# Kernel tuning notes

Hardware: AMD Instinct MI355X
Metric: run time of the kernel (lower is better)

Reference implementation:

```python
import jax, jax.numpy as jnp
import numpy as np

B, D, H, F, L, M, MEM, ACT, STO, HID = 2048, 1024, 8, 4096, 2, 256, 16, 32, 1024, 1024
HD = D // H
SCALE = HD ** -0.5
EPS = 1e-4


def rmsnorm(x, w):
    return x * jax.lax.rsqrt(jnp.mean(x * x, axis=-1, keepdims=True) + EPS) * w


def setup_inputs() -> dict:
    key = jax.random.key(0)
    ks = iter(jax.random.split(key, 32))

    def nrm(shape, scale=0.02):
        return jax.random.normal(next(ks), shape, dtype=jnp.float32) * scale

    return {
        'stoch': jax.random.normal(next(ks), (B, STO), dtype=jnp.float32),
        'deter': jax.random.normal(next(ks), (B, D), dtype=jnp.float32),
        'action': jax.random.normal(next(ks), (B, ACT), dtype=jnp.float32),
        'memory': jax.random.normal(next(ks), (B, MEM, D), dtype=jnp.float32),
        'inp_w1': nrm((STO + ACT, HID)), 'inp_b1': jnp.zeros((HID,), jnp.float32),
        'inp_nw': jnp.ones((HID,), jnp.float32),
        'inp_w2': nrm((HID, D)), 'inp_b2': jnp.zeros((D,), jnp.float32),
        'Wq': nrm((L, D, D)), 'bq': jnp.zeros((L, D), jnp.float32),
        'Wk': nrm((L, D, D)), 'bk': jnp.zeros((L, D), jnp.float32),
        'Wv': nrm((L, D, D)), 'bv': jnp.zeros((L, D), jnp.float32),
        'Wo': nrm((L, D, D)), 'bo': jnp.zeros((L, D), jnp.float32),
        'rel_emb': nrm((L, 2 * M + 1, H)),
        'n1w': jnp.ones((L, D), jnp.float32), 'n2w': jnp.ones((L, D), jnp.float32),
        'ffw1': nrm((L, D, F)), 'ffb1': jnp.zeros((L, F), jnp.float32),
        'ffw2': nrm((L, F, D)), 'ffb2': jnp.zeros((L, D), jnp.float32),
        'fnw': jnp.ones((D,), jnp.float32),
    }


def reference(stoch, deter, action, memory, inp_w1, inp_b1, inp_nw, inp_w2, inp_b2,
              Wq, bq, Wk, bk, Wv, bv, Wo, bo, rel_emb, n1w, n2w,
              ffw1, ffb1, ffw2, ffb2, fnw):
    # action normalization: denominator is detached in torch
    a = action / jax.lax.stop_gradient(jnp.maximum(jnp.abs(action), 1.0))
    tok = jnp.concatenate([stoch.reshape(stoch.shape[0], -1), a], axis=-1)
    tok = jax.nn.silu(rmsnorm(tok @ inp_w1 + inp_b1, inp_nw)) @ inp_w2 + inp_b2  # [B,D]
    seq = jnp.concatenate([memory, tok[:, None, :]], axis=1)  # [B,S,D], S = MEM+1
    S = seq.shape[1]
    rel = jnp.clip(jnp.arange(S)[:, None] - jnp.arange(S)[None, :], -M, M) + M  # [S,S]
    for l in range(L):
        xn = rmsnorm(seq, n1w[l])
        q = (xn @ Wq[l] + bq[l]).reshape(-1, S, H, HD)
        k = (xn @ Wk[l] + bk[l]).reshape(-1, S, H, HD)
        v = (xn @ Wv[l] + bv[l]).reshape(-1, S, H, HD)
        bias = rel_emb[l][rel].transpose(2, 0, 1)  # [H,S,S]
        scores = jnp.einsum('bqhd,bkhd->bhqk', q, k) * SCALE + bias[None]
        probs = jax.nn.softmax(scores, axis=-1)
        att = jnp.einsum('bhqk,bkhd->bqhd', probs, v).reshape(-1, S, D)
        seq = seq + (att @ Wo[l] + bo[l])
        xn2 = rmsnorm(seq, n2w[l])
        seq = seq + (jax.nn.gelu(xn2 @ ffw1[l] + ffb1[l], approximate=False) @ ffw2[l] + ffb2[l])
    new_deter = rmsnorm(seq[:, -1] + deter, fnw)
    new_mem = jax.lax.stop_gradient(seq[:, -MEM:])
    return (new_deter, new_mem)
```

## Files before the change

### kernel.cpp

```cpp
#include <hip/hip_runtime.h>
#include <hip/hip_bf16.h>
#include <math.h>

#define NB 2048
#define ND 1024
#define NH 8
#define NHD 128
#define NF 4096
#define NL 2
#define NMEM 16
#define NS 17
#define NROWS (NB*NS)
#define NTOK 1056
#define SCALE_ATT 0.08838834764831845f

typedef unsigned short u16;
typedef unsigned int u32;

typedef __bf16 bf16x8 __attribute__((ext_vector_type(8)));
typedef float f32x4 __attribute__((ext_vector_type(4)));

__device__ __forceinline__ float bf2f(u16 h) {
  union { u32 u; float f; } c; c.u = ((u32)h) << 16; return c.f;
}
__device__ __forceinline__ u16 f2bf(float f) {
  union { float ff; u32 u; } c; c.ff = f;
  return (u16)((c.u + 0x7FFFu + ((c.u >> 16) & 1u)) >> 16);
}
__device__ __forceinline__ bf16x8 as_b8(uint4 u) {
  union { uint4 u; bf16x8 b; } c; c.u = u; return c.b;
}

__device__ __forceinline__ void gload16(const void* g, void* l) {
  __builtin_amdgcn_global_load_lds(
      (const __attribute__((address_space(1))) void*)(uintptr_t)g,
      (__attribute__((address_space(3))) void*)(u32)(uintptr_t)l,
      16, 0, 0);
}

__device__ __forceinline__ void pack_tile(const float* __restrict__ src,
                                          u16* __restrict__ dst,
                                          int K, int N, int n0, int k0,
                                          float* tile )
{
  int tx = threadIdx.x & 31, ty = threadIdx.x >> 5;
#pragma unroll
  for (int r = ty; r < 32; r += 8)
    tile[r * 33 + tx] = src[(size_t)(k0 + r) * N + n0 + tx];
  __syncthreads();
#pragma unroll
  for (int r = ty; r < 32; r += 8)
    dst[(size_t)(n0 + r) * K + k0 + tx] = f2bf(tile[tx * 33 + r]);
}

__global__ __launch_bounds__(256)
void pack_wT_k(const float* __restrict__ src, u16* __restrict__ dst, int K, int N)
{
  __shared__ float tile[32 * 33];
  pack_tile(src, dst, K, N, blockIdx.x * 32, blockIdx.y * 32, tile);
}

__global__ __launch_bounds__(256)
void pack_layer_k(const float* __restrict__ wq, const float* __restrict__ wk,
                  const float* __restrict__ wv, const float* __restrict__ wo,
                  const float* __restrict__ w1, const float* __restrict__ w2,
                  const float* __restrict__ bq, const float* __restrict__ bk,
                  const float* __restrict__ bv,
                  u16* __restrict__ qkvT, u16* __restrict__ oT,
                  u16* __restrict__ f1T, u16* __restrict__ f2T,
                  float* __restrict__ BQKV)
{
  __shared__ float tile[32 * 33];
  int id = blockIdx.x;
  if (id < 4096) {
    int which = id >> 10, l = id & 1023;
    const float* src = which == 0 ? wq : which == 1 ? wk : which == 2 ? wv : wo;
    u16* dst = which == 3 ? oT : qkvT + (size_t)which * 1048576;
    pack_tile(src, dst, 1024, 1024, (l & 31) * 32, (l >> 5) * 32, tile);
  } else if (id < 8192) {
    int l = id - 4096;
    pack_tile(w1, f1T, 1024, 4096, (l & 127) * 32, (l >> 7) * 32, tile);
  } else if (id < 12288) {
    int l = id - 8192;
    pack_tile(w2, f2T, 4096, 1024, (l & 31) * 32, (l >> 5) * 32, tile);
  } else {
    int j = (id - 12288) * 256 + threadIdx.x;
    if (j < 3072)
      BQKV[j] = (j < 1024) ? bq[j] : (j < 2048 ? bk[j - 1024] : bv[j - 2048]);
  }
}

template<int EPI>
__global__ __launch_bounds__(256)
void gemm2_k(const u16* __restrict__ A, int lda,
             const u16* __restrict__ BT, int ldb,
             const float* __restrict__ bias,
             u16* __restrict__ Cb, float* __restrict__ Cf, int ldc,
             int K)
{
  __shared__ __align__(16) u16 Asm[2][128 * 32];
  __shared__ __align__(16) u16 Bsm[2][128 * 32];
  const int tid  = threadIdx.x;
  const int lane = tid & 63;
  const int wv   = tid >> 6;
  const int wm   = wv >> 1, wn = wv & 1;
  const int lr   = lane & 15;
  const int kb   = lane >> 4;

  const int gx = gridDim.x;
  const int nwg = gx * gridDim.y;
  int bid = blockIdx.y * gx + blockIdx.x;
  if ((nwg & 7) == 0) bid = (bid & 7) * (nwg >> 3) + (bid >> 3);
  const int bx = bid % gx, by = bid / gx;
  const long bmBase = (long)by * 128;
  const int  bnBase = bx * 128;

  const int srow = tid >> 2;
  const int skc  = ((tid & 3) ^ ((srow >> 1) & 3)) * 8;
  const u16* aG0 = A  + (size_t)(bmBase + srow) * lda + skc;
  const u16* aG1 = aG0 + (size_t)64 * lda;
  const u16* bG0 = BT + (size_t)(bnBase + srow) * ldb + skc;
  const u16* bG1 = bG0 + (size_t)64 * ldb;
  const int wbase = (tid & ~63) * 8;
  const int rslot = (kb ^ ((lr >> 1) & 3)) * 8;

  f32x4 acc[4][4];
#pragma unroll
  for (int m = 0; m < 4; ++m)
#pragma unroll
    for (int n = 0; n < 4; ++n)
      acc[m][n] = (f32x4){0.0f, 0.0f, 0.0f, 0.0f};

  const int nk = K >> 5;
  {
    u16* aL = &Asm[0][wbase];
    u16* bL = &Bsm[0][wbase];
    gload16(aG0, aL);
    gload16(aG1, aL + 2048);
    gload16(bG0, bL);
    gload16(bG1, bL + 2048);
  }
  asm volatile("s_waitcnt vmcnt(0)" ::: "memory");
  __builtin_amdgcn_s_barrier();

  for (int i = 0; i < nk; ++i) {
    const int cur = i & 1;
    if (i + 1 < nk) {
      const int kt = (i + 1) << 5;
      u16* aL = &Asm[cur ^ 1][wbase];
      u16* bL = &Bsm[cur ^ 1][wbase];
      gload16(aG0 + kt, aL);
      gload16(aG1 + kt, aL + 2048);
      gload16(bG0 + kt, bL);
      gload16(bG1 + kt, bL + 2048);
    }
    bf16x8 af[4], bfv[4];
#pragma unroll
    for (int m = 0; m < 4; ++m)
      af[m] = as_b8(*(const uint4*)&Asm[cur][(wm * 64 + m * 16 + lr) * 32 + rslot]);
#pragma unroll
    for (int n = 0; n < 4; ++n)
      bfv[n] = as_b8(*(const uint4*)&Bsm[cur][(wn * 64 + n * 16 + lr) * 32 + rslot]);
#pragma unroll
    for (int m = 0; m < 4; ++m)
#pragma unroll
      for (int n = 0; n < 4; ++n)
        acc[m][n] = __builtin_amdgcn_mfma_f32_16x16x32_bf16(af[m], bfv[n], acc[m][n], 0, 0, 0);
    asm volatile("s_waitcnt vmcnt(0)" ::: "memory");
    __builtin_amdgcn_s_barrier();
  }

#pragma unroll
  for (int m = 0; m < 4; ++m) {
#pragma unroll
    for (int n = 0; n < 4; ++n) {
      int gcol = bnBase + wn * 64 + n * 16 + lr;
      float bv = bias[gcol];
      long growb = bmBase + wm * 64 + m * 16 + (lane >> 4) * 4;
#pragma unroll
      for (int i = 0; i < 4; ++i) {
        float val = acc[m][n][i] + bv;
        long row = growb + i;
        if (EPI == 1) val = 0.5f * val * (1.0f + erff(val * 0.70710678118654752f));
        if (EPI == 0 || EPI == 1) {
          Cb[(size_t)row * ldc + gcol] = f2bf(val);
        } else if (EPI == 2) {
          float* p = Cf + (size_t)row * ldc + gcol;
          *p = *p + val;
        } else {
          Cf[(size_t)row * ldc + gcol] = val;
        }
      }
    }
  }
}

__global__ __launch_bounds__(256)
void prep_tokcat_k(const float* __restrict__ stoch, const float* __restrict__ action,
                   u16* __restrict__ tok)
{
  size_t idx = (size_t)blockIdx.x * 256 + threadIdx.x;
  if (idx >= (size_t)NB * NTOK) return;
  int b = (int)(idx / NTOK), j = (int)(idx % NTOK);
  float v;
  if (j < 1024) {
    v = stoch[(size_t)b * 1024 + j];
  } else {
    float a = action[(size_t)b * 32 + (j - 1024)];
    v = a / fmaxf(fabsf(a), 1.0f);
  }
  tok[idx] = f2bf(v);
}

__global__ __launch_bounds__(256)
void rmsnorm_f32_k(const float* __restrict__ X, const float* __restrict__ w,
                   u16* __restrict__ Y)
{
  const int wv = threadIdx.x >> 6, lane = threadIdx.x & 63;
  const size_t row = (size_t)blockIdx.x * 4 + wv;
  const float* x = X + row * 1024 + lane * 16;
  float4 v[4];
#pragma unroll
  for (int j = 0; j < 4; ++j) v[j] = ((const float4*)x)[j];
  float ss = 0.0f;
#pragma unroll
  for (int j = 0; j < 4; ++j)
    ss += v[j].x * v[j].x + v[j].y * v[j].y + v[j].z * v[j].z + v[j].w * v[j].w;
#pragma unroll
  for (int o = 1; o < 64; o <<= 1) ss += __shfl_xor(ss, o, 64);
  const float r = rsqrtf(ss * (1.0f / 1024.0f) + 1e-4f);
  const float* wp = w + lane * 16;
  union { u16 s[16]; uint4 u[2]; } ob;
#pragma unroll
  for (int j = 0; j < 4; ++j) {
    float4 wj = ((const float4*)wp)[j];
    ob.s[j * 4 + 0] = f2bf(v[j].x * r * wj.x);
    ob.s[j * 4 + 1] = f2bf(v[j].y * r * wj.y);
    ob.s[j * 4 + 2] = f2bf(v[j].z * r * wj.z);
    ob.s[j * 4 + 3] = f2bf(v[j].w * r * wj.w);
  }
  uint4* dst = (uint4*)(Y + row * 1024 + lane * 16);
  dst[0] = ob.u[0];
  dst[1] = ob.u[1];
}

__global__ __launch_bounds__(256)
void rmsnorm_silu_k(u16* __restrict__ X, const float* __restrict__ w)
{
  const int wv = threadIdx.x >> 6, lane = threadIdx.x & 63;
  const size_t row = (size_t)blockIdx.x * 4 + wv;
  u16* x = X + row * 1024 + lane * 16;
  union { u16 s[16]; uint4 u[2]; } iv;
  iv.u[0] = ((const uint4*)x)[0];
  iv.u[1] = ((const uint4*)x)[1];
  float f[16];
  float ss = 0.0f;
#pragma unroll
  for (int j = 0; j < 16; ++j) { f[j] = bf2f(iv.s[j]); ss += f[j] * f[j]; }
#pragma unroll
  for (int o = 1; o < 64; o <<= 1) ss += __shfl_xor(ss, o, 64);
  const float r = rsqrtf(ss * (1.0f / 1024.0f) + 1e-4f);
  const float* wp = w + lane * 16;
  union { u16 s[16]; uint4 u[2]; } ob;
#pragma unroll
  for (int j = 0; j < 16; ++j) {
    float n = f[j] * r * wp[j];
    ob.s[j] = f2bf(n / (1.0f + expf(-n)));
  }
  ((uint4*)x)[0] = ob.u[0];
  ((uint4*)x)[1] = ob.u[1];
}

__global__ __launch_bounds__(256)
void init_seq_k(const float* __restrict__ mem, float* __restrict__ seq)
{
  size_t idx = ((size_t)blockIdx.x * 256 + threadIdx.x) * 4;
  if (idx >= (size_t)NB * 16 * 1024) return;
  size_t b = idx / (16 * 1024), rem = idx % (16 * 1024);
  float4 v = *(const float4*)&mem[idx];
  *(float4*)&seq[b * (size_t)NS * 1024 + rem] = v;
}

__global__ __launch_bounds__(256)
void copy_mem_k(const float* __restrict__ seq, float* __restrict__ out)
{
  size_t idx = ((size_t)blockIdx.x * 256 + threadIdx.x) * 4;
  if (idx >= (size_t)NB * 16 * 1024) return;
  size_t b = idx / (16 * 1024), rem = idx % (16 * 1024);
  float4 v = *(const float4*)&seq[b * (size_t)NS * 1024 + 1024 + rem];
  *(float4*)&out[idx] = v;
}

__global__ __launch_bounds__(256)
void final_deter_k(const float* __restrict__ seq, const float* __restrict__ deter,
                   const float* __restrict__ fnw, float* __restrict__ out)
{
  int b = blockIdx.x;
  const float* xs = seq + ((size_t)b * NS + 16) * 1024;
  const float* dt = deter + (size_t)b * 1024;
  int t = threadIdx.x;
  float v[4];
#pragma unroll
  for (int j = 0; j < 4; ++j) v[j] = xs[t * 4 + j] + dt[t * 4 + j];
  float ss = v[0] * v[0] + v[1] * v[1] + v[2] * v[2] + v[3] * v[3];
#pragma unroll
  for (int o = 1; o < 64; o <<= 1) ss += __shfl_xor(ss, o, 64);
  __shared__ float red[4];
  if ((t & 63) == 0) red[t >> 6] = ss;
  __syncthreads();
  float tot = red[0] + red[1] + red[2] + red[3];
  float r = rsqrtf(tot * (1.0f / 1024.0f) + 1e-4f);
  float4 ov;
  ov.x = v[0] * r * fnw[t * 4 + 0];
  ov.y = v[1] * r * fnw[t * 4 + 1];
  ov.z = v[2] * r * fnw[t * 4 + 2];
  ov.w = v[3] * r * fnw[t * 4 + 3];
  *(float4*)&out[(size_t)b * 1024 + t * 4] = ov;
}

#define LSTR 132
__global__ __launch_bounds__(256)
void attn_k(const u16* __restrict__ QKV, const float* __restrict__ rel,
            u16* __restrict__ O)
{
  __shared__ float qs[NS * LSTR];
  __shared__ float ks[NS * LSTR];
  __shared__ float vs[NS * LSTR];
  __shared__ float sc[NS * 20];
  int bh = blockIdx.x;
  int b = bh >> 3, h = bh & 7;
  int t = threadIdx.x;
  const size_t rowb = (size_t)b * NS * 3072 + h * 128;
  for (int e = t; e < NS * 16; e += 256) {
    int i = e >> 4, d = (e & 15) * 8;
    size_t off = rowb + (size_t)i * 3072 + d;
    uint4 q4 = *(const uint4*)(QKV + off);
    uint4 k4 = *(const uint4*)(QKV + off + 1024);
    uint4 v4 = *(const uint4*)(QKV + off + 2048);
    const u16* qp = (const u16*)&q4;
    const u16* kp = (const u16*)&k4;
    const u16* vp = (const u16*)&v4;
#pragma unroll
    for (int j = 0; j < 8; ++j) {
      qs[i * LSTR + d + j] = bf2f(qp[j]);
      ks[i * LSTR + d + j] = bf2f(kp[j]);
      vs[i * LSTR + d + j] = bf2f(vp[j]);
    }
  }
  __syncthreads();
  for (int e = t; e < NS * NS; e += 256) {
    int i = e / NS, j = e % NS;
    const float4* q4 = (const float4*)&qs[i * LSTR];
    const float4* k4 = (const float4*)&ks[j * LSTR];
    float s = 0.0f;
#pragma unroll
    for (int dd = 0; dd < 32; ++dd) {
      float4 a = q4[dd], bb = k4[dd];
      s += a.x * bb.x + a.y * bb.y + a.z * bb.z + a.w * bb.w;
    }
    sc[i * 20 + j] = s * SCALE_ATT + rel[(i - j + 256) * 8 + h];
  }
  __syncthreads();
  if (t < NS) {
    float mx = -1e30f;
    for (int j = 0; j < NS; ++j) mx = fmaxf(mx, sc[t * 20 + j]);
    float sum = 0.0f;
    for (int j = 0; j < NS; ++j) { float e = expf(sc[t * 20 + j] - mx); sc[t * 20 + j] = e; sum += e; }
    float inv = 1.0f / sum;
    for (int j = 0; j < NS; ++j) sc[t * 20 + j] *= inv;
  }
  __syncthreads();
  const size_t obase = (size_t)b * NS * 1024 + h * 128;
  for (int e = t; e < NS * 128; e += 256) {
    int i = e >> 7, d = e & 127;
    float o = 0.0f;
#pragma unroll
    for (int j = 0; j < NS; ++j) o += sc[i * 20 + j] * vs[j * LSTR + d];
    O[obase + (size_t)i * 1024 + d] = f2bf(o);
  }
}

extern "C" void kernel_launch(void* const* d_in, const int* in_sizes, int n_in,
                              void* d_out, int out_size, void* d_ws, size_t ws_size,
                              hipStream_t stream)
{
  const float* stoch  = (const float*)d_in[0];
  const float* deter  = (const float*)d_in[1];
  const float* action = (const float*)d_in[2];
  const float* memory = (const float*)d_in[3];
  const float* inp_w1 = (const float*)d_in[4];
  const float* inp_b1 = (const float*)d_in[5];
  const float* inp_nw = (const float*)d_in[6];
  const float* inp_w2 = (const float*)d_in[7];
  const float* inp_b2 = (const float*)d_in[8];
  const float* Wq = (const float*)d_in[9];
  const float* bq = (const float*)d_in[10];
  const float* Wk = (const float*)d_in[11];
  const float* bk = (const float*)d_in[12];
  const float* Wv = (const float*)d_in[13];
  const float* bv = (const float*)d_in[14];
  const float* Wo = (const float*)d_in[15];
  const float* bo = (const float*)d_in[16];
  const float* rel_emb = (const float*)d_in[17];
  const float* n1w = (const float*)d_in[18];
  const float* n2w = (const float*)d_in[19];
  const float* ffw1 = (const float*)d_in[20];
  const float* ffb1 = (const float*)d_in[21];
  const float* ffw2 = (const float*)d_in[22];
  const float* ffb2 = (const float*)d_in[23];
  const float* fnw  = (const float*)d_in[24];
  float* out = (float*)d_out;

  char* ws = (char*)d_ws;
  float* SEQ = (float*)ws;
  u16* XN  = (u16*)(ws + 142606336ULL);
  u16* QKV = (u16*)(ws + 213909504ULL);
  u16* FFH = QKV;
  u16* TOK = (u16*)(ws + 427819008ULL);
  u16* H1  = (u16*)(ws + 432144384ULL);
  u16* PK  = (u16*)(ws + 436338688ULL);
  float* BQKV = (float*)(ws + 461504512ULL);
  if (ws_size < 461516800ULL) return;

  dim3 blk(256);

  u16* w1T = PK;
  u16* w2T = PK + 1024 * 1056;
  pack_wT_k<<<dim3(1024 / 32, 1056 / 32), blk, 0, stream>>>(inp_w1, w1T, NTOK, 1024);
  pack_wT_k<<<dim3(1024 / 32, 1024 / 32), blk, 0, stream>>>(inp_w2, w2T, 1024, 1024);
  prep_tokcat_k<<<(NB * NTOK + 255) / 256, blk, 0, stream>>>(stoch, action, TOK);
  gemm2_k<0><<<dim3(8, 16), blk, 0, stream>>>(TOK, NTOK, w1T, NTOK, inp_b1, H1, nullptr, 1024, NTOK);
  rmsnorm_silu_k<<<NB / 4, blk, 0, stream>>>(H1, inp_nw);
  gemm2_k<3><<<dim3(8, 16), blk, 0, stream>>>(H1, 1024, w2T, 1024, inp_b2, nullptr, SEQ + 16 * 1024, NS * 1024, 1024);
  init_seq_k<<<(NB * 16 * 1024 / 4 + 255) / 256, blk, 0, stream>>>(memory, SEQ);

  u16* qkvT = PK;
  u16* oT  = PK + 3145728;
  u16* f1T = PK + 4194304;
  u16* f2T = PK + 8388608;

  for (int l = 0; l < NL; ++l) {
    const float* wq = Wq + (size_t)l * ND * ND;
    const float* wk = Wk + (size_t)l * ND * ND;
    const float* wv = Wv + (size_t)l * ND * ND;
    const float* wo = Wo + (size_t)l * ND * ND;
    const float* w1 = ffw1 + (size_t)l * ND * NF;
    const float* w2 = ffw2 + (size_t)l * NF * ND;
    const float* rl = rel_emb + (size_t)l * 513 * NH;

    pack_layer_k<<<12300, blk, 0, stream>>>(wq, wk, wv, wo, w1, w2,
                                            bq + l * ND, bk + l * ND, bv + l * ND,
                                            qkvT, oT, f1T, f2T, BQKV);

    rmsnorm_f32_k<<<NROWS / 4, blk, 0, stream>>>(SEQ, n1w + l * ND, XN);
    gemm2_k<0><<<dim3(24, 272), blk, 0, stream>>>(XN, 1024, qkvT, 1024, BQKV, QKV, nullptr, 3072, 1024);
    attn_k<<<NB * NH, blk, 0, stream>>>(QKV, rl, XN);
    gemm2_k<2><<<dim3(8, 272), blk, 0, stream>>>(XN, 1024, oT, 1024, bo + l * ND, nullptr, SEQ, 1024, 1024);
    rmsnorm_f32_k<<<NROWS / 4, blk, 0, stream>>>(SEQ, n2w + l * ND, XN);
    for (int c = 0; c < 2; ++c) {
      size_t r0 = (size_t)c * 17408;
      gemm2_k<1><<<dim3(32, 136), blk, 0, stream>>>(XN + r0 * 1024, 1024, f1T, 1024, ffb1 + l * NF, FFH, nullptr, 4096, 1024);
      gemm2_k<2><<<dim3(8, 136), blk, 0, stream>>>(FFH, 4096, f2T, 4096, ffb2 + l * ND, nullptr, SEQ + r0 * 1024, 1024, 4096);
    }
  }

  final_deter_k<<<NB, blk, 0, stream>>>(SEQ, deter, fnw, out);
  copy_mem_k<<<(NB * 16 * 1024 / 4 + 255) / 256, blk, 0, stream>>>(SEQ, out + (size_t)NB * ND);
}
```

Before: 3.401 ms.

## Switch GEMM to 32x32x16 MFMA tiles and use fast exp/tanh GELU

Result: slower. 3.490 ms (+2.6%).

```diff
diff --git a/kernel.cpp b/kernel.cpp
--- a/kernel.cpp
+++ b/kernel.cpp
@@ -19,6 +19,7 @@
 
 typedef __bf16 bf16x8 __attribute__((ext_vector_type(8)));
 typedef float f32x4 __attribute__((ext_vector_type(4)));
+typedef float f32x16 __attribute__((ext_vector_type(16)));
 
 __device__ __forceinline__ float bf2f(u16 h) {
   union { u32 u; float f; } c; c.u = ((u32)h) << 16; return c.f;
@@ -36,6 +37,11 @@
       (const __attribute__((address_space(1))) void*)(uintptr_t)g,
       (__attribute__((address_space(3))) void*)(u32)(uintptr_t)l,
       16, 0, 0);
+}
+
+__device__ __forceinline__ float gelu_fast(float x) {
+  float u = x * (0.7978845608f + 0.0356774081f * x * x);
+  return x * (1.0f / (1.0f + __expf(-2.0f * u)));
 }
 
 __device__ __forceinline__ void pack_tile(const float* __restrict__ src,
@@ -104,8 +110,8 @@
   const int lane = tid & 63;
   const int wv   = tid >> 6;
   const int wm   = wv >> 1, wn = wv & 1;
-  const int lr   = lane & 15;
-  const int kb   = lane >> 4;
+  const int lr32 = lane & 31;
+  const int half = lane >> 5;
 
   const int gx = gridDim.x;
   const int nwg = gx * gridDim.y;
@@ -122,14 +128,16 @@
   const u16* bG0 = BT + (size_t)(bnBase + srow) * ldb + skc;
   const u16* bG1 = bG0 + (size_t)64 * ldb;
   const int wbase = (tid & ~63) * 8;
-  const int rslot = (kb ^ ((lr >> 1) & 3)) * 8;
-
-  f32x4 acc[4][4];
-#pragma unroll
-  for (int m = 0; m < 4; ++m)
-#pragma unroll
-    for (int n = 0; n < 4; ++n)
-      acc[m][n] = (f32x4){0.0f, 0.0f, 0.0f, 0.0f};
+
+  const int rsl0 = ((0 * 2 + half) ^ ((lane >> 1) & 3)) * 8;
+  const int rsl1 = ((1 * 2 + half) ^ ((lane >> 1) & 3)) * 8;
+
+  f32x16 acc[2][2];
+#pragma unroll
+  for (int m = 0; m < 2; ++m)
+#pragma unroll
+    for (int n = 0; n < 2; ++n)
+      acc[m][n] = (f32x16)(0.0f);
 
   const int nk = K >> 5;
   {
@@ -154,34 +162,42 @@
       gload16(bG0 + kt, bL);
       gload16(bG1 + kt, bL + 2048);
     }
-    bf16x8 af[4], bfv[4];
-#pragma unroll
-    for (int m = 0; m < 4; ++m)
-      af[m] = as_b8(*(const uint4*)&Asm[cur][(wm * 64 + m * 16 + lr) * 32 + rslot]);
-#pragma unroll
-    for (int n = 0; n < 4; ++n)
-      bfv[n] = as_b8(*(const uint4*)&Bsm[cur][(wn * 64 + n * 16 + lr) * 32 + rslot]);
-#pragma unroll
-    for (int m = 0; m < 4; ++m)
-#pragma unroll
-      for (int n = 0; n < 4; ++n)
-        acc[m][n] = __builtin_amdgcn_mfma_f32_16x16x32_bf16(af[m], bfv[n], acc[m][n], 0, 0, 0);
+    bf16x8 af[2][2], bf[2][2];
+#pragma unroll
+    for (int m = 0; m < 2; ++m) {
+      const int ar = (wm * 64 + m * 32 + lr32) * 32;
+      af[m][0] = as_b8(*(const uint4*)&Asm[cur][ar + rsl0]);
+      af[m][1] = as_b8(*(const uint4*)&Asm[cur][ar + rsl1]);
+    }
+#pragma unroll
+    for (int n = 0; n < 2; ++n) {
+      const int br = (wn * 64 + n * 32 + lr32) * 32;
+      bf[n][0] = as_b8(*(const uint4*)&Bsm[cur][br + rsl0]);
+      bf[n][1] = as_b8(*(const uint4*)&Bsm[cur][br + rsl1]);
+    }
+#pragma unroll
+    for (int ks = 0; ks < 2; ++ks)
+#pragma unroll
+      for (int m = 0; m < 2; ++m)
+#pragma unroll
+        for (int n = 0; n < 2; ++n)
+          acc[m][n] = __builtin_amdgcn_mfma_f32_32x32x16_bf16(af[m][ks], bf[n][ks], acc[m][n], 0, 0, 0);
     asm volatile("s_waitcnt vmcnt(0)" ::: "memory");
     __builtin_amdgcn_s_barrier();
   }
 
 #pragma unroll
-  for (int m = 0; m < 4; ++m) {
-#pragma unroll
-    for (int n = 0; n < 4; ++n) {
-      int gcol = bnBase + wn * 64 + n * 16 + lr;
+  for (int m = 0; m < 2; ++m) {
+#pragma unroll
+    for (int n = 0; n < 2; ++n) {
+      int gcol = bnBase + wn * 64 + n * 32 + lr32;
       float bv = bias[gcol];
-      long growb = bmBase + wm * 64 + m * 16 + (lane >> 4) * 4;
-#pragma unroll
-      for (int i = 0; i < 4; ++i) {
-        float val = acc[m][n][i] + bv;
-        long row = growb + i;
-        if (EPI == 1) val = 0.5f * val * (1.0f + erff(val * 0.70710678118654752f));
+      long rowbase = bmBase + wm * 64 + m * 32 + 4 * half;
+#pragma unroll
+      for (int reg = 0; reg < 16; ++reg) {
+        long row = rowbase + (reg & 3) + 8 * (reg >> 2);
+        float val = acc[m][n][reg] + bv;
+        if (EPI == 1) val = gelu_fast(val);
         if (EPI == 0 || EPI == 1) {
           Cb[(size_t)row * ldc + gcol] = f2bf(val);
         } else if (EPI == 2) {
@@ -265,7 +281,7 @@
 #pragma unroll
   for (int j = 0; j < 16; ++j) {
     float n = f[j] * r * wp[j];
-    ob.s[j] = f2bf(n / (1.0f + expf(-n)));
+    ob.s[j] = f2bf(n / (1.0f + __expf(-n)));
   }
   ((uint4*)x)[0] = ob.u[0];
   ((uint4*)x)[1] = ob.u[1];
@@ -365,7 +381,7 @@
     float mx = -1e30f;
     for (int j = 0; j < NS; ++j) mx = fmaxf(mx, sc[t * 20 + j]);
     float sum = 0.0f;
-    for (int j = 0; j < NS; ++j) { float e = expf(sc[t * 20 + j] - mx); sc[t * 20 + j] = e; sum += e; }
+    for (int j = 0; j < NS; ++j) { float e = __expf(sc[t * 20 + j] - mx); sc[t * 20 + j] = e; sum += e; }
     float inv = 1.0f / sum;
     for (int j = 0; j < NS; ++j) sc[t * 20 + j] *= inv;
   }
```

## Store residual stream in bf16 and use fast GELU/exp approximations

Applied to the files above, without the earlier changes.

Measured after the change: 3.107 ms. -8.7%, faster.

```diff
diff --git a/kernel.cpp b/kernel.cpp
--- a/kernel.cpp
+++ b/kernel.cpp
@@ -36,6 +36,11 @@
       (const __attribute__((address_space(1))) void*)(uintptr_t)g,
       (__attribute__((address_space(3))) void*)(u32)(uintptr_t)l,
       16, 0, 0);
+}
+
+__device__ __forceinline__ float gelu_fast(float x) {
+  float u = x * (0.7978845608f + 0.0356774081f * x * x);
+  return x * (1.0f / (1.0f + __expf(-2.0f * u)));
 }
 
 __device__ __forceinline__ void pack_tile(const float* __restrict__ src,
@@ -95,7 +100,7 @@
 void gemm2_k(const u16* __restrict__ A, int lda,
              const u16* __restrict__ BT, int ldb,
              const float* __restrict__ bias,
-             u16* __restrict__ Cb, float* __restrict__ Cf, int ldc,
+             u16* __restrict__ Cb, int ldc,
              int K)
 {
   __shared__ __align__(16) u16 Asm[2][128 * 32];
@@ -181,15 +186,10 @@
       for (int i = 0; i < 4; ++i) {
         float val = acc[m][n][i] + bv;
         long row = growb + i;
-        if (EPI == 1) val = 0.5f * val * (1.0f + erff(val * 0.70710678118654752f));
-        if (EPI == 0 || EPI == 1) {
-          Cb[(size_t)row * ldc + gcol] = f2bf(val);
-        } else if (EPI == 2) {
-          float* p = Cf + (size_t)row * ldc + gcol;
-          *p = *p + val;
-        } else {
-          Cf[(size_t)row * ldc + gcol] = val;
-        }
+        u16* p = Cb + (size_t)row * ldc + gcol;
+        if (EPI == 1) val = gelu_fast(val);
+        if (EPI == 2) val += bf2f(*p);
+        *p = f2bf(val);
       }
     }
   }
@@ -213,32 +213,26 @@
 }
 
 __global__ __launch_bounds__(256)
-void rmsnorm_f32_k(const float* __restrict__ X, const float* __restrict__ w,
-                   u16* __restrict__ Y)
+void rmsnorm_bf16_k(const u16* __restrict__ X, const float* __restrict__ w,
+                    u16* __restrict__ Y)
 {
   const int wv = threadIdx.x >> 6, lane = threadIdx.x & 63;
   const size_t row = (size_t)blockIdx.x * 4 + wv;
-  const float* x = X + row * 1024 + lane * 16;
-  float4 v[4];
-#pragma unroll
-  for (int j = 0; j < 4; ++j) v[j] = ((const float4*)x)[j];
+  const u16* x = X + row * 1024 + lane * 16;
+  union { u16 s[16]; uint4 u[2]; } iv;
+  iv.u[0] = ((const uint4*)x)[0];
+  iv.u[1] = ((const uint4*)x)[1];
+  float f[16];
   float ss = 0.0f;
 #pragma unroll
-  for (int j = 0; j < 4; ++j)
-    ss += v[j].x * v[j].x + v[j].y * v[j].y + v[j].z * v[j].z + v[j].w * v[j].w;
+  for (int j = 0; j < 16; ++j) { f[j] = bf2f(iv.s[j]); ss += f[j] * f[j]; }
 #pragma unroll
   for (int o = 1; o < 64; o <<= 1) ss += __shfl_xor(ss, o, 64);
   const float r = rsqrtf(ss * (1.0f / 1024.0f) + 1e-4f);
   const float* wp = w + lane * 16;
   union { u16 s[16]; uint4 u[2]; } ob;
 #pragma unroll
-  for (int j = 0; j < 4; ++j) {
-    float4 wj = ((const float4*)wp)[j];
-    ob.s[j * 4 + 0] = f2bf(v[j].x * r * wj.x);
-    ob.s[j * 4 + 1] = f2bf(v[j].y * r * wj.y);
-    ob.s[j * 4 + 2] = f2bf(v[j].z * r * wj.z);
-    ob.s[j * 4 + 3] = f2bf(v[j].w * r * wj.w);
-  }
+  for (int j = 0; j < 16; ++j) ob.s[j] = f2bf(f[j] * r * wp[j]);
   uint4* dst = (uint4*)(Y + row * 1024 + lane * 16);
   dst[0] = ob.u[0];
   dst[1] = ob.u[1];
@@ -265,43 +259,54 @@
 #pragma unroll
   for (int j = 0; j < 16; ++j) {
     float n = f[j] * r * wp[j];
-    ob.s[j] = f2bf(n / (1.0f + expf(-n)));
+    ob.s[j] = f2bf(n / (1.0f + __expf(-n)));
   }
   ((uint4*)x)[0] = ob.u[0];
   ((uint4*)x)[1] = ob.u[1];
 }
 
 __global__ __launch_bounds__(256)
-void init_seq_k(const float* __restrict__ mem, float* __restrict__ seq)
-{
-  size_t idx = ((size_t)blockIdx.x * 256 + threadIdx.x) * 4;
+void init_seq_k(const float* __restrict__ mem, u16* __restrict__ seq)
+{
+  size_t idx = ((size_t)blockIdx.x * 256 + threadIdx.x) * 8;
   if (idx >= (size_t)NB * 16 * 1024) return;
   size_t b = idx / (16 * 1024), rem = idx % (16 * 1024);
-  float4 v = *(const float4*)&mem[idx];
-  *(float4*)&seq[b * (size_t)NS * 1024 + rem] = v;
-}
-
-__global__ __launch_bounds__(256)
-void copy_mem_k(const float* __restrict__ seq, float* __restrict__ out)
-{
-  size_t idx = ((size_t)blockIdx.x * 256 + threadIdx.x) * 4;
+  float4 v0 = *(const float4*)&mem[idx];
+  float4 v1 = *(const float4*)&mem[idx + 4];
+  union { u16 s[8]; uint4 u; } ob;
+  ob.s[0] = f2bf(v0.x); ob.s[1] = f2bf(v0.y); ob.s[2] = f2bf(v0.z); ob.s[3] = f2bf(v0.w);
+  ob.s[4] = f2bf(v1.x); ob.s[5] = f2bf(v1.y); ob.s[6] = f2bf(v1.z); ob.s[7] = f2bf(v1.w);
+  *(uint4*)&seq[b * (size_t)NS * 1024 + rem] = ob.u;
+}
+
+__global__ __launch_bounds__(256)
+void copy_mem_k(const u16* __restrict__ seq, float* __restrict__ out)
+{
+  size_t idx = ((size_t)blockIdx.x * 256 + threadIdx.x) * 8;
   if (idx >= (size_t)NB * 16 * 1024) return;
   size_t b = idx / (16 * 1024), rem = idx % (16 * 1024);
-  float4 v = *(const float4*)&seq[b * (size_t)NS * 1024 + 1024 + rem];
-  *(float4*)&out[idx] = v;
-}
-
-__global__ __launch_bounds__(256)
-void final_deter_k(const float* __restrict__ seq, const float* __restrict__ deter,
+  union { u16 s[8]; uint4 u; } iv;
+  iv.u = *(const uint4*)&seq[b * (size_t)NS * 1024 + 1024 + rem];
+  float4 o0, o1;
+  o0.x = bf2f(iv.s[0]); o0.y = bf2f(iv.s[1]); o0.z = bf2f(iv.s[2]); o0.w = bf2f(iv.s[3]);
+  o1.x = bf2f(iv.s[4]); o1.y = bf2f(iv.s[5]); o1.z = bf2f(iv.s[6]); o1.w = bf2f(iv.s[7]);
+  *(float4*)&out[idx] = o0;
+  *(float4*)&out[idx + 4] = o1;
+}
+
+__global__ __launch_bounds__(256)
+void final_deter_k(const u16* __restrict__ seq, const float* __restrict__ deter,
                    const float* __restrict__ fnw, float* __restrict__ out)
 {
   int b = blockIdx.x;
-  const float* xs = seq + ((size_t)b * NS + 16) * 1024;
+  const u16* xs = seq + ((size_t)b * NS + 16) * 1024;
   const float* dt = deter + (size_t)b * 1024;
   int t = threadIdx.x;
+  union { u16 s[4]; uint2 u; } iv;
+  iv.u = *(const uint2*)&xs[t * 4];
   float v[4];
 #pragma unroll
-  for (int j = 0; j < 4; ++j) v[j] = xs[t * 4 + j] + dt[t * 4 + j];
+  for (int j = 0; j < 4; ++j) v[j] = bf2f(iv.s[j]) + dt[t * 4 + j];
   float ss = v[0] * v[0] + v[1] * v[1] + v[2] * v[2] + v[3] * v[3];
 #pragma unroll
   for (int o = 1; o < 64; o <<= 1) ss += __shfl_xor(ss, o, 64);
@@ -365,7 +370,7 @@
     float mx = -1e30f;
     for (int j = 0; j < NS; ++j) mx = fmaxf(mx, sc[t * 20 + j]);
     float sum = 0.0f;
-    for (int j = 0; j < NS; ++j) { float e = expf(sc[t * 20 + j] - mx); sc[t * 20 + j] = e; sum += e; }
+    for (int j = 0; j < NS; ++j) { float e = __expf(sc[t * 20 + j] - mx); sc[t * 20 + j] = e; sum += e; }
     float inv = 1.0f / sum;
     for (int j = 0; j < NS; ++j) sc[t * 20 + j] *= inv;
   }
@@ -412,15 +417,15 @@
   float* out = (float*)d_out;
 
   char* ws = (char*)d_ws;
-  float* SEQ = (float*)ws;
-  u16* XN  = (u16*)(ws + 142606336ULL);
-  u16* QKV = (u16*)(ws + 213909504ULL);
+  u16* SEQ = (u16*)ws;
+  u16* XN  = (u16*)(ws + 71303168ULL);
+  u16* QKV = (u16*)(ws + 142606336ULL);
   u16* FFH = QKV;
-  u16* TOK = (u16*)(ws + 427819008ULL);
-  u16* H1  = (u16*)(ws + 432144384ULL);
-  u16* PK  = (u16*)(ws + 436338688ULL);
-  float* BQKV = (float*)(ws + 461504512ULL);
-  if (ws_size < 461516800ULL) return;
+  u16* TOK = (u16*)(ws + 356515840ULL);
+  u16* H1  = (u16*)(ws + 360841216ULL);
+  u16* PK  = (u16*)(ws + 365035520ULL);
+  float* BQKV = (float*)(ws + 390201344ULL);
+  if (ws_size < 390213632ULL) return;
 
   dim3 blk(256);
 
@@ -429,10 +434,10 @@
   pack_wT_k<<<dim3(1024 / 32, 1056 / 32), blk, 0, stream>>>(inp_w1, w1T, NTOK, 1024);
   pack_wT_k<<<dim3(1024 / 32, 1024 / 32), blk, 0, stream>>>(inp_w2, w2T, 1024, 1024);
   prep_tokcat_k<<<(NB * NTOK + 255) / 256, blk, 0, stream>>>(stoch, action, TOK);
-  gemm2_k<0><<<dim3(8, 16), blk, 0, stream>>>(TOK, NTOK, w1T, NTOK, inp_b1, H1, nullptr, 1024, NTOK);
+  gemm2_k<0><<<dim3(8, 16), blk, 0, stream>>>(TOK, NTOK, w1T, NTOK, inp_b1, H1, 1024, NTOK);
   rmsnorm_silu_k<<<NB / 4, blk, 0, stream>>>(H1, inp_nw);
-  gemm2_k<3><<<dim3(8, 16), blk, 0, stream>>>(H1, 1024, w2T, 1024, inp_b2, nullptr, SEQ + 16 * 1024, NS * 1024, 1024);
-  init_seq_k<<<(NB * 16 * 1024 / 4 + 255) / 256, blk, 0, stream>>>(memory, SEQ);
+  gemm2_k<0><<<dim3(8, 16), blk, 0, stream>>>(H1, 1024, w2T, 1024, inp_b2, SEQ + 16 * 1024, NS * 1024, 1024);
+  init_seq_k<<<(NB * 16 * 1024 / 8 + 255) / 256, blk, 0, stream>>>(memory, SEQ);
 
   u16* qkvT = PK;
   u16* oT  = PK + 3145728;
@@ -452,18 +457,18 @@
                                             bq + l * ND, bk + l * ND, bv + l * ND,
                                             qkvT, oT, f1T, f2T, BQKV);
 
-    rmsnorm_f32_k<<<NROWS / 4, blk, 0, stream>>>(SEQ, n1w + l * ND, XN);
-    gemm2_k<0><<<dim3(24, 272), blk, 0, stream>>>(XN, 1024, qkvT, 1024, BQKV, QKV, nullptr, 3072, 1024);
+    rmsnorm_bf16_k<<<NROWS / 4, blk, 0, stream>>>(SEQ, n1w + l * ND, XN);
+    gemm2_k<0><<<dim3(24, 272), blk, 0, stream>>>(XN, 1024, qkvT, 1024, BQKV, QKV, 3072, 1024);
     attn_k<<<NB * NH, blk, 0, stream>>>(QKV, rl, XN);
-    gemm2_k<2><<<dim3(8, 272), blk, 0, stream>>>(XN, 1024, oT, 1024, bo + l * ND, nullptr, SEQ, 1024, 1024);
-    rmsnorm_f32_k<<<NROWS / 4, blk, 0, stream>>>(SEQ, n2w + l * ND, XN);
+    gemm2_k<2><<<dim3(8, 272), blk, 0, stream>>>(XN, 1024, oT, 1024, bo + l * ND, SEQ, 1024, 1024);
+    rmsnorm_bf16_k<<<NROWS / 4, blk, 0, stream>>>(SEQ, n2w + l * ND, XN);
     for (int c = 0; c < 2; ++c) {
       size_t r0 = (size_t)c * 17408;
-      gemm2_k<1><<<dim3(32, 136), blk, 0, stream>>>(XN + r0 * 1024, 1024, f1T, 1024, ffb1 + l * NF, FFH, nullptr, 4096, 1024);
-      gemm2_k<2><<<dim3(8, 136), blk, 0, stream>>>(FFH, 4096, f2T, 4096, ffb2 + l * ND, nullptr, SEQ + r0 * 1024, 1024, 4096);
+      gemm2_k<1><<<dim3(32, 136), blk, 0, stream>>>(XN + r0 * 1024, 1024, f1T, 1024, ffb1 + l * NF, FFH, 4096, 1024);
+      gemm2_k<2><<<dim3(8, 136), blk, 0, stream>>>(FFH, 4096, f2T, 4096, ffb2 + l * ND, SEQ + r0 * 1024, 1024, 4096);
     }
   }
 
   final_deter_k<<<NB, blk, 0, stream>>>(SEQ, deter, fnw, out);
-  copy_mem_k<<<(NB * 16 * 1024 / 4 + 255) / 256, blk, 0, stream>>>(SEQ, out + (size_t)NB * ND);
-}
+  copy_mem_k<<<(NB * 16 * 1024 / 8 + 255) / 256, blk, 0, stream>>>(SEQ, out + (size_t)NB * ND);
+}
```
